# Performance work log

Measured on AMD Instinct MI355X. Metric: run time of the kernel, lower is better.

The kernel has to match this reference:

```python
import jax, jax.numpy as jnp
import numpy as np

B, S, D, E, H, K = 4, 2048, 1024, 8, 4096, 2
EPS = 1e-6


def _ln(x, scale, bias):
    m = jnp.mean(x, axis=-1, keepdims=True)
    v = jnp.mean(jnp.square(x - m), axis=-1, keepdims=True)
    return (x - m) * jax.lax.rsqrt(v + EPS) * scale + bias


def setup_inputs() -> dict:
    key = jax.random.key(0)
    ks = jax.random.split(key, 4)
    s1 = 1.0 / np.sqrt(D)
    s2 = 1.0 / np.sqrt(H)
    return {
        "x": jax.random.normal(ks[0], (B, S, D), jnp.float32),
        "router_ln_scale": jnp.ones((D,), jnp.float32),
        "router_ln_bias": jnp.zeros((D,), jnp.float32),
        "router_w": jax.random.normal(ks[1], (E, D), jnp.float32) * s1,
        "router_b": jnp.zeros((E,), jnp.float32),
        "expert_ln_scale": jnp.ones((E, D), jnp.float32),
        "expert_ln_bias": jnp.zeros((E, D), jnp.float32),
        "w1": jax.random.normal(ks[2], (E, H, D), jnp.float32) * s1,
        "b1": jnp.zeros((E, H), jnp.float32),
        "w2": jax.random.normal(ks[3], (E, D, H), jnp.float32) * s2,
        "b2": jnp.zeros((E, D), jnp.float32),
    }


def reference(x, router_ln_scale, router_ln_bias, router_w, router_b,
              expert_ln_scale, expert_ln_bias, w1, b1, w2, b2):
    orig_shape = x.shape
    xf = x.reshape(-1, D)                       # [T, D]
    T = xf.shape[0]

    # Router: LayerNorm -> Linear -> softmax -> top-k, renormalize weights
    logits = _ln(xf, router_ln_scale, router_ln_bias) @ router_w.T + router_b
    probs = jax.nn.softmax(logits, axis=-1)     # [T, E]
    topw, topi = jax.lax.top_k(probs, K)        # [T, K]
    topw = topw / jnp.sum(topw, axis=-1, keepdims=True)
    # Dense gate matrix: weight for unrouted (token, expert) pairs is 0,
    # matching the original scatter-combine math exactly.
    gates = jnp.zeros((T, E), xf.dtype).at[jnp.arange(T)[:, None], topi].set(topw)

    # Expert MLP: LayerNorm -> fc1 -> GELU(exact) -> fc2, vmapped over experts
    def expert(ls, lb, W1, B1, W2, B2):
        h = jax.nn.gelu(_ln(xf, ls, lb) @ W1.T + B1, approximate=False)
        return h @ W2.T + B2                    # [T, D]

    ys = jax.vmap(expert)(expert_ln_scale, expert_ln_bias, w1, b1, w2, b2)  # [E, T, D]
    out = jnp.einsum('te,etd->td', gates, ys)
    return out.reshape(orig_shape)
```

## Files before the change

kernel.cpp:

```cpp
#include <hip/hip_runtime.h>
#include <hip/hip_bf16.h>

#define TT 8192
#define DD 1024
#define EE 8
#define HH 4096
#define SLOTS 16384
#define SLOTSP (SLOTS + 256)
#define MAXRT1 (SLOTS / 128 + EE)
#define NRB 2048
#define NWB 2048

typedef __bf16 bf16x8 __attribute__((ext_vector_type(8)));
typedef float f32x4 __attribute__((ext_vector_type(4)));

__device__ __forceinline__ float bf2f(unsigned u) { return __uint_as_float(u << 16); }
__device__ __forceinline__ unsigned short f2bf(float f) {
  __hip_bfloat16 h = __float2bfloat16(f);
  return __builtin_bit_cast(unsigned short, h);
}
__device__ __forceinline__ f32x4 MF(bf16x8 a, bf16x8 b, f32x4 c) {
  return __builtin_amdgcn_mfma_f32_16x16x32_bf16(a, b, c, 0, 0, 0);
}


__global__ __launch_bounds__(256) void k_fused_rw(
    const float* __restrict__ x, const float* __restrict__ rls,
    const float* __restrict__ rlb, const float* __restrict__ rw,
    const float* __restrict__ rb, const float* __restrict__ w1,
    const float* __restrict__ w2, unsigned short* __restrict__ xhat,
    int* __restrict__ topk, float* __restrict__ gates, int* __restrict__ ranks,
    int* __restrict__ blkcnt, unsigned short* __restrict__ w1b,
    unsigned short* __restrict__ w2b) {
  if (blockIdx.x >= NRB) {
    const size_t n4t = (size_t)2 * EE * HH * DD / 4;
    const size_t n4w1 = (size_t)EE * HH * DD / 4;
    size_t i = (size_t)(blockIdx.x - NRB) * 256 + threadIdx.x;
    const size_t stride = (size_t)NWB * 256;
    for (; i < n4t; i += stride) {
      const float4* src; unsigned short* dst; size_t j;
      if (i < n4w1) { src = (const float4*)w1; dst = w1b; j = i; }
      else          { src = (const float4*)w2; dst = w2b; j = i - n4w1; }
      float4 v = src[j];
      ushort4 ov;
      ov.x = f2bf(v.x); ov.y = f2bf(v.y); ov.z = f2bf(v.z); ov.w = f2bf(v.w);
      ((ushort4*)dst)[j] = ov;
    }
    return;
  }
  const int tid = threadIdx.x, lane = tid & 63, v = tid >> 6;
  const int t = blockIdx.x * 4 + v;
  __shared__ int sh_e[4][2];
  const float4* xr = (const float4*)(x + (size_t)t * DD);
  float4 xv[4];
#pragma unroll
  for (int j = 0; j < 4; ++j) xv[j] = xr[lane + 64 * j];
  float s = 0.f, s2 = 0.f;
#pragma unroll
  for (int j = 0; j < 4; ++j) {
    s += xv[j].x + xv[j].y + xv[j].z + xv[j].w;
    s2 += xv[j].x * xv[j].x + xv[j].y * xv[j].y + xv[j].z * xv[j].z + xv[j].w * xv[j].w;
  }
#pragma unroll
  for (int o = 32; o > 0; o >>= 1) { s += __shfl_xor(s, o); s2 += __shfl_xor(s2, o); }
  const float mean = s * (1.0f / DD);
  const float var = s2 * (1.0f / DD) - mean * mean;
  const float inv = rsqrtf(var + 1e-6f);
  float xh[4][4];
  unsigned short* xo = xhat + (size_t)t * DD;
#pragma unroll
  for (int j = 0; j < 4; ++j) {
    xh[j][0] = (xv[j].x - mean) * inv; xh[j][1] = (xv[j].y - mean) * inv;
    xh[j][2] = (xv[j].z - mean) * inv; xh[j][3] = (xv[j].w - mean) * inv;
    ushort4 pk;
    pk.x = f2bf(xh[j][0]); pk.y = f2bf(xh[j][1]);
    pk.z = f2bf(xh[j][2]); pk.w = f2bf(xh[j][3]);
    ((ushort4*)xo)[lane + 64 * j] = pk;
  }
  float r[4][4];
#pragma unroll
  for (int j = 0; j < 4; ++j) {
    float4 sc = ((const float4*)rls)[lane + 64 * j];
    float4 bi = ((const float4*)rlb)[lane + 64 * j];
    r[j][0] = fmaf(xh[j][0], sc.x, bi.x); r[j][1] = fmaf(xh[j][1], sc.y, bi.y);
    r[j][2] = fmaf(xh[j][2], sc.z, bi.z); r[j][3] = fmaf(xh[j][3], sc.w, bi.w);
  }
  float pe[EE];
#pragma unroll
  for (int e = 0; e < EE; ++e) {
    float acc = 0.f;
#pragma unroll
    for (int j = 0; j < 4; ++j) {
      float4 w = ((const float4*)(rw + (size_t)e * DD))[lane + 64 * j];
      acc = fmaf(r[j][0], w.x, fmaf(r[j][1], w.y, fmaf(r[j][2], w.z, fmaf(r[j][3], w.w, acc))));
    }
    pe[e] = acc;
  }
#pragma unroll
  for (int o = 32; o > 0; o >>= 1) {
#pragma unroll
    for (int e = 0; e < EE; ++e) pe[e] += __shfl_xor(pe[e], o);
  }
  int i1 = 0, i2 = -1;
  if (lane == 0) {
    float lg[EE];
    for (int e = 0; e < EE; ++e) lg[e] = pe[e] + rb[e];
    for (int e = 1; e < EE; ++e) if (lg[e] > lg[i1]) i1 = e;
    for (int e = 0; e < EE; ++e) { if (e == i1) continue; if (i2 < 0 || lg[e] > lg[i2]) i2 = e; }
    float eb = expf(lg[i2] - lg[i1]);
    float den = 1.0f / (1.0f + eb);
    topk[t] = i1 | (i2 << 8);
    gates[2 * t] = den;
    gates[2 * t + 1] = eb * den;
    sh_e[v][0] = i1; sh_e[v][1] = i2;
  }
  __syncthreads();
  if (lane == 0) {
    int r0 = 0, r1 = 0;
    for (int q = 0; q < 2 * v; ++q) {
      int ee = sh_e[q >> 1][q & 1];
      r0 += (ee == i1); r1 += (ee == i2);
    }
    ranks[2 * t] = r0;
    ranks[2 * t + 1] = r1;
  }
  if (tid < EE) {
    int c = 0;
    for (int q = 0; q < 8; ++q) c += (sh_e[q >> 1][q & 1] == tid);
    blkcnt[blockIdx.x * EE + tid] = c;
  }
}

__global__ __launch_bounds__(256) void k_offsets(int* __restrict__ ctrl,
                                                 int* __restrict__ blkcnt) {
  __shared__ int chunk[32 * EE];
  __shared__ int tot[EE];
  const int t = threadIdx.x, e = t & 7, c = t >> 3;
  int s = 0;
  for (int i = 0; i < 64; ++i) s += blkcnt[(c * 64 + i) * EE + e];
  chunk[c * EE + e] = s;
  __syncthreads();
  if (t < EE) {
    int run = 0;
    for (int c2 = 0; c2 < 32; ++c2) { int vv = chunk[c2 * EE + t]; chunk[c2 * EE + t] = run; run += vv; }
    tot[t] = run;
    ctrl[t] = run;
  }
  __syncthreads();
  if (t == 0) {
    int o = 0, rr = 0;
    ctrl[8] = 0; ctrl[25] = 0;
    for (int e2 = 0; e2 < EE; ++e2) {
      int cc = tot[e2];
      o += cc; ctrl[9 + e2] = o;
      rr += (cc + 127) >> 7; ctrl[26 + e2] = rr;
    }
  }
  int run = chunk[c * EE + e];
  for (int i = 0; i < 64; ++i) {
    int idx = (c * 64 + i) * EE + e;
    int vv = blkcnt[idx];
    blkcnt[idx] = run;
    run += vv;
  }
}

__global__ __launch_bounds__(256) void k_build(
    const unsigned short* __restrict__ xhat, const float* __restrict__ els,
    const float* __restrict__ elb, const int* __restrict__ ctrl,
    const int* __restrict__ topk, const int* __restrict__ ranks,
    const int* __restrict__ blkbase, unsigned short* __restrict__ A,
    int* __restrict__ tok_pos) {
  int p = blockIdx.x * 2 + (threadIdx.x >> 7);
  int t = p >> 1, k = p & 1, tid = threadIdx.x & 127;
  int e = (topk[t] >> (k * 8)) & 0xff;
  int pos = ctrl[8 + e] + blkbase[(p >> 3) * EE + e] + ranks[p];
  if (tid == 0) tok_pos[p] = pos;
  int i = tid * 8;
  uint4 xv = *(const uint4*)(xhat + (size_t)t * DD + i);
  const float* sp = els + (size_t)e * DD + i;
  const float* bp = elb + (size_t)e * DD + i;
  float4 s0 = *(const float4*)sp, s1 = *(const float4*)(sp + 4);
  float4 b0 = *(const float4*)bp, b1 = *(const float4*)(bp + 4);
  unsigned r0 = (unsigned)f2bf(fmaf(bf2f(xv.x & 0xffffu), s0.x, b0.x)) |
                ((unsigned)f2bf(fmaf(bf2f(xv.x >> 16), s0.y, b0.y)) << 16);
  unsigned r1 = (unsigned)f2bf(fmaf(bf2f(xv.y & 0xffffu), s0.z, b0.z)) |
                ((unsigned)f2bf(fmaf(bf2f(xv.y >> 16), s0.w, b0.w)) << 16);
  unsigned r2 = (unsigned)f2bf(fmaf(bf2f(xv.z & 0xffffu), s1.x, b1.x)) |
                ((unsigned)f2bf(fmaf(bf2f(xv.z >> 16), s1.y, b1.y)) << 16);
  unsigned r3 = (unsigned)f2bf(fmaf(bf2f(xv.w & 0xffffu), s1.z, b1.z)) |
                ((unsigned)f2bf(fmaf(bf2f(xv.w >> 16), s1.w, b1.w)) << 16);
  uint4 ov; ov.x = r0; ov.y = r1; ov.z = r2; ov.w = r3;
  *(uint4*)(A + (size_t)pos * DD + i) = ov;
}

#define GLL(S, D)                                                              \
  __builtin_amdgcn_global_load_lds(                                            \
      (const __attribute__((address_space(1))) unsigned int*)(S),              \
      (__attribute__((address_space(3))) unsigned int*)(D), 16, 0, 0)
#define STAGE(P, KT) do {                                                      \
    const unsigned short* sA_ = pA + (size_t)(KT) * 32;                        \
    const unsigned short* sB_ = pB + (size_t)(KT) * 32;                        \
    char* dA_ = sL + (P) * 16384;                                              \
    char* dB_ = dA_ + 8192;                                                    \
    GLL(sA_, dA_); GLL(sA_ + 16 * KDIM, dA_ + 1024);                           \
    GLL(sB_, dB_); GLL(sB_ + 16 * KDIM, dB_ + 1024);                           \
  } while (0)

template <int KDIM, bool GELU>
__global__ __launch_bounds__(256, 3) void k_gemm4(
    const unsigned short* __restrict__ Amat,
    const unsigned short* __restrict__ W,
    const float* __restrict__ bias,
    unsigned short* __restrict__ Outm,
    const int* __restrict__ ctrl, int NTOT) {
  constexpr int NT = KDIM / 32;
  __shared__ __align__(16) char smem[32768];
  const int* rtp = ctrl + 25;

  const int nwg = gridDim.x * gridDim.y;
  const int lin = blockIdx.y * gridDim.x + blockIdx.x;
  const int xcd = lin & 7, loc = lin >> 3;
  const int q = nwg >> 3, rr = nwg & 7;
  const int lin2 = (xcd < rr ? xcd * (q + 1) : rr * (q + 1) + (xcd - rr) * q) + loc;
  const int by = lin2 % gridDim.y;
  const int bx = lin2 / gridDim.y;
  if (bx >= rtp[EE]) return;
  int e = 0;
  while (bx >= rtp[e + 1]) ++e;
  const int rt = bx - rtp[e];
  const int row0 = ctrl[8 + e] + rt * 128;
  int vrows = ctrl[e] - rt * 128;
  if (vrows > 128) vrows = 128;
  const int n0 = by * 128;

  const int tid = threadIdx.x, lane = tid & 63, w = tid >> 6;
  const int wr = w >> 1, wc = w & 1;

  const int u = (lane * 16) ^ (((lane >> 5) & 1) << 5);
  const int ri = u >> 6;
  const int ci = (u & 63) >> 1;
  const unsigned short* pA = Amat + (size_t)(row0 + 32 * w + ri) * KDIM + ci;
  const unsigned short* pB = W + ((size_t)e * NTOT + n0 + 32 * w + ri) * KDIM + ci;
  char* sL = smem + (2 * w) * 1024 + lane * 16;

  const int lt = (((lane & 15) << 6) | ((lane >> 4) << 4)) ^ (((lane >> 3) & 1) << 5);

  f32x4 acc[4][4];
#pragma unroll
  for (int m = 0; m < 4; ++m)
#pragma unroll
    for (int n = 0; n < 4; ++n) acc[m][n] = (f32x4){0.f, 0.f, 0.f, 0.f};

  bf16x8 a[4], b[4];

  STAGE(0, 0);
  __syncthreads();

  for (int kt = 0; kt < NT; ++kt) {
    const int p = kt & 1;
    if (kt + 1 < NT) STAGE(p ^ 1, kt + 1);
    const char* ab = smem + p * 16384 + wr * 4096 + lt;
    const char* bb = smem + p * 16384 + 8192 + wc * 4096 + lt;
#pragma unroll
    for (int m = 0; m < 4; ++m) a[m] = *(const bf16x8*)(ab + m * 1024);
#pragma unroll
    for (int n = 0; n < 4; ++n) b[n] = *(const bf16x8*)(bb + n * 1024);
#pragma unroll
    for (int m = 0; m < 4; ++m)
#pragma unroll
      for (int n = 0; n < 4; ++n)
        acc[m][n] = MF(a[m], b[n], acc[m][n]);
    __syncthreads();
  }

#pragma unroll
  for (int m = 0; m < 4; ++m) {
    const int rbase = wr * 64 + m * 16 + (lane >> 4) * 4;
#pragma unroll
    for (int n = 0; n < 4; ++n) {
      const int col = n0 + wc * 64 + n * 16 + (lane & 15);
      const float bv_ = bias[(size_t)e * NTOT + col];
#pragma unroll
      for (int j = 0; j < 4; ++j) {
        const int r = rbase + j;
        if (r < vrows) {
          float vv = acc[m][n][j] + bv_;
          if constexpr (GELU) vv = 0.5f * vv * (1.0f + erff(vv * 0.70710678f));
          Outm[(size_t)(row0 + r) * NTOT + col] = f2bf(vv);
        }
      }
    }
  }
}

__global__ __launch_bounds__(256) void k_combine(
    const unsigned short* __restrict__ Y, const int* __restrict__ tok_pos,
    const float* __restrict__ gates, float* __restrict__ out) {
  int t = blockIdx.x, tid = threadIdx.x;
  int p0 = tok_pos[2 * t], p1 = tok_pos[2 * t + 1];
  float g0 = gates[2 * t], g1 = gates[2 * t + 1];
  ushort4 y0 = ((const ushort4*)(Y + (size_t)p0 * DD))[tid];
  ushort4 y1 = ((const ushort4*)(Y + (size_t)p1 * DD))[tid];
  float4 o;
  o.x = g0 * bf2f(y0.x) + g1 * bf2f(y1.x);
  o.y = g0 * bf2f(y0.y) + g1 * bf2f(y1.y);
  o.z = g0 * bf2f(y0.z) + g1 * bf2f(y1.z);
  o.w = g0 * bf2f(y0.w) + g1 * bf2f(y1.w);
  ((float4*)(out + (size_t)t * DD))[tid] = o;
}

__global__ __launch_bounds__(256) void k_sentinel(float* out, int n) {
  int i = blockIdx.x * 256 + threadIdx.x;
  if (i < n) out[i] = 12345.0f;
}

extern "C" void kernel_launch(void* const* d_in, const int* in_sizes, int n_in,
                              void* d_out, int out_size, void* d_ws, size_t ws_size,
                              hipStream_t stream) {
  const float* x   = (const float*)d_in[0];
  const float* rls = (const float*)d_in[1];
  const float* rlb = (const float*)d_in[2];
  const float* rw  = (const float*)d_in[3];
  const float* rb  = (const float*)d_in[4];
  const float* els = (const float*)d_in[5];
  const float* elb = (const float*)d_in[6];
  const float* w1  = (const float*)d_in[7];
  const float* b1  = (const float*)d_in[8];
  const float* w2  = (const float*)d_in[9];
  const float* b2  = (const float*)d_in[10];
  float* out = (float*)d_out;

  char* wsb = (char*)d_ws;
  size_t o = 0;
  int* ctrl = (int*)(wsb + o);                    o += 256;
  int* tok_pos = (int*)(wsb + o);                 o += (size_t)SLOTS * 4;
  float* gates = (float*)(wsb + o);               o += (size_t)SLOTS * 4;
  int* topk = (int*)(wsb + o);                    o += (size_t)TT * 4;
  int* ranks = (int*)(wsb + o);                   o += (size_t)SLOTS * 4;
  int* blkcnt = (int*)(wsb + o);                  o += (size_t)NRB * EE * 4;
  unsigned short* xhat = (unsigned short*)(wsb + o); o += (size_t)TT * DD * 2;
  unsigned short* Abuf = (unsigned short*)(wsb + o); o += (size_t)SLOTSP * DD * 2;
  unsigned short* w1b = (unsigned short*)(wsb + o);  o += (size_t)EE * HH * DD * 2;
  unsigned short* w2b = (unsigned short*)(wsb + o);  o += (size_t)EE * DD * HH * 2;
  unsigned short* Hm = (unsigned short*)(wsb + o);   o += (size_t)SLOTSP * HH * 2;
  unsigned short* Yb = (unsigned short*)(wsb + o);   o += (size_t)SLOTS * DD * 2;

  if (ws_size < o) {
    k_sentinel<<<(out_size + 255) / 256, 256, 0, stream>>>(out, out_size);
    return;
  }

  k_fused_rw<<<NRB + NWB, 256, 0, stream>>>(x, rls, rlb, rw, rb, w1, w2, xhat,
                                            topk, gates, ranks, blkcnt, w1b, w2b);
  k_offsets<<<1, 256, 0, stream>>>(ctrl, blkcnt);
  k_build<<<SLOTS / 2, 256, 0, stream>>>(xhat, els, elb, ctrl, topk, ranks,
                                         blkcnt, Abuf, tok_pos);
  k_gemm4<DD, true><<<dim3(MAXRT1, HH / 128), 256, 0, stream>>>(Abuf, w1b, b1, Hm, ctrl, HH);
  k_gemm4<HH, false><<<dim3(MAXRT1, DD / 128), 256, 0, stream>>>(Hm, w2b, b2, Yb, ctrl, DD);
  k_combine<<<TT, 256, 0, stream>>>(Yb, tok_pos, gates, out);
}
```

Measured before the change: 571.2 us.

## Split-K the second expert GEMM and raster GEMM tiles in 8x8 groups

The fc2 GEMM (K=4096) is split into two K-halves via blockIdx.z. Each half writes its own bf16 partial output slice, with the bias added only in slice 0, and the combine kernel sums both partials before applying the gates. Both GEMMs also remap block indices into 8x8 tile groups, so neighbouring workgroups share A and W tiles in cache. This gives the fc2 GEMM more blocks to balance across CUs and shortens each block's K loop. The cost is twice the Y write/read traffic, a larger workspace, and an extra bf16 rounding of the partial sums.

```diff
diff --git a/kernel.cpp b/kernel.cpp
--- a/kernel.cpp
+++ b/kernel.cpp
@@ -207,24 +207,27 @@
     GLL(sB_, dB_); GLL(sB_ + 16 * KDIM, dB_ + 1024);                           \
   } while (0)
 
-template <int KDIM, bool GELU>
+template <int KDIM, int NTILES, bool GELU>
 __global__ __launch_bounds__(256, 3) void k_gemm4(
     const unsigned short* __restrict__ Amat,
     const unsigned short* __restrict__ W,
     const float* __restrict__ bias,
     unsigned short* __restrict__ Outm,
-    const int* __restrict__ ctrl, int NTOT) {
-  constexpr int NT = KDIM / 32;
+    const int* __restrict__ ctrl, int NTOT, size_t outSlice) {
   __shared__ __align__(16) char smem[32768];
   const int* rtp = ctrl + 25;
+  const int z = blockIdx.z;
+  const int kt0 = z * NTILES;
 
   const int nwg = gridDim.x * gridDim.y;
   const int lin = blockIdx.y * gridDim.x + blockIdx.x;
   const int xcd = lin & 7, loc = lin >> 3;
   const int q = nwg >> 3, rr = nwg & 7;
   const int lin2 = (xcd < rr ? xcd * (q + 1) : rr * (q + 1) + (xcd - rr) * q) + loc;
-  const int by = lin2 % gridDim.y;
-  const int bx = lin2 / gridDim.y;
+  const int tXc = gridDim.x >> 3;
+  const int chunk = lin2 >> 6, win = lin2 & 63;
+  const int bx = (chunk % tXc) * 8 + (win & 7);
+  const int by = (chunk / tXc) * 8 + (win >> 3);
   if (bx >= rtp[EE]) return;
   int e = 0;
   while (bx >= rtp[e + 1]) ++e;
@@ -254,12 +257,12 @@
 
   bf16x8 a[4], b[4];
 
-  STAGE(0, 0);
+  STAGE(0, kt0);
   __syncthreads();
 
-  for (int kt = 0; kt < NT; ++kt) {
-    const int p = kt & 1;
-    if (kt + 1 < NT) STAGE(p ^ 1, kt + 1);
+  for (int it = 0; it < NTILES; ++it) {
+    const int p = it & 1;
+    if (it + 1 < NTILES) STAGE(p ^ 1, kt0 + it + 1);
     const char* ab = smem + p * 16384 + wr * 4096 + lt;
     const char* bb = smem + p * 16384 + 8192 + wc * 4096 + lt;
 #pragma unroll
@@ -274,20 +277,21 @@
     __syncthreads();
   }
 
+  unsigned short* outz = Outm + (size_t)z * outSlice;
 #pragma unroll
   for (int m = 0; m < 4; ++m) {
     const int rbase = wr * 64 + m * 16 + (lane >> 4) * 4;
 #pragma unroll
     for (int n = 0; n < 4; ++n) {
       const int col = n0 + wc * 64 + n * 16 + (lane & 15);
-      const float bv_ = bias[(size_t)e * NTOT + col];
+      const float bv_ = (z == 0) ? bias[(size_t)e * NTOT + col] : 0.0f;
 #pragma unroll
       for (int j = 0; j < 4; ++j) {
         const int r = rbase + j;
         if (r < vrows) {
           float vv = acc[m][n][j] + bv_;
           if constexpr (GELU) vv = 0.5f * vv * (1.0f + erff(vv * 0.70710678f));
-          Outm[(size_t)(row0 + r) * NTOT + col] = f2bf(vv);
+          outz[(size_t)(row0 + r) * NTOT + col] = f2bf(vv);
         }
       }
     }
@@ -300,13 +304,16 @@
   int t = blockIdx.x, tid = threadIdx.x;
   int p0 = tok_pos[2 * t], p1 = tok_pos[2 * t + 1];
   float g0 = gates[2 * t], g1 = gates[2 * t + 1];
-  ushort4 y0 = ((const ushort4*)(Y + (size_t)p0 * DD))[tid];
-  ushort4 y1 = ((const ushort4*)(Y + (size_t)p1 * DD))[tid];
+  const unsigned short* Y1 = Y + (size_t)SLOTSP * DD;
+  ushort4 a0 = ((const ushort4*)(Y + (size_t)p0 * DD))[tid];
+  ushort4 a1 = ((const ushort4*)(Y1 + (size_t)p0 * DD))[tid];
+  ushort4 c0 = ((const ushort4*)(Y + (size_t)p1 * DD))[tid];
+  ushort4 c1 = ((const ushort4*)(Y1 + (size_t)p1 * DD))[tid];
   float4 o;
-  o.x = g0 * bf2f(y0.x) + g1 * bf2f(y1.x);
-  o.y = g0 * bf2f(y0.y) + g1 * bf2f(y1.y);
-  o.z = g0 * bf2f(y0.z) + g1 * bf2f(y1.z);
-  o.w = g0 * bf2f(y0.w) + g1 * bf2f(y1.w);
+  o.x = g0 * (bf2f(a0.x) + bf2f(a1.x)) + g1 * (bf2f(c0.x) + bf2f(c1.x));
+  o.y = g0 * (bf2f(a0.y) + bf2f(a1.y)) + g1 * (bf2f(c0.y) + bf2f(c1.y));
+  o.z = g0 * (bf2f(a0.z) + bf2f(a1.z)) + g1 * (bf2f(c0.z) + bf2f(c1.z));
+  o.w = g0 * (bf2f(a0.w) + bf2f(a1.w)) + g1 * (bf2f(c0.w) + bf2f(c1.w));
   ((float4*)(out + (size_t)t * DD))[tid] = o;
 }
 
@@ -344,7 +351,7 @@
   unsigned short* w1b = (unsigned short*)(wsb + o);  o += (size_t)EE * HH * DD * 2;
   unsigned short* w2b = (unsigned short*)(wsb + o);  o += (size_t)EE * DD * HH * 2;
   unsigned short* Hm = (unsigned short*)(wsb + o);   o += (size_t)SLOTSP * HH * 2;
-  unsigned short* Yb = (unsigned short*)(wsb + o);   o += (size_t)SLOTS * DD * 2;
+  unsigned short* Yb = (unsigned short*)(wsb + o);   o += (size_t)2 * SLOTSP * DD * 2;
 
   if (ws_size < o) {
     k_sentinel<<<(out_size + 255) / 256, 256, 0, stream>>>(out, out_size);
@@ -356,7 +363,9 @@
   k_offsets<<<1, 256, 0, stream>>>(ctrl, blkcnt);
   k_build<<<SLOTS / 2, 256, 0, stream>>>(xhat, els, elb, ctrl, topk, ranks,
                                          blkcnt, Abuf, tok_pos);
-  k_gemm4<DD, true><<<dim3(MAXRT1, HH / 128), 256, 0, stream>>>(Abuf, w1b, b1, Hm, ctrl, HH);
-  k_gemm4<HH, false><<<dim3(MAXRT1, DD / 128), 256, 0, stream>>>(Hm, w2b, b2, Yb, ctrl, DD);
+  k_gemm4<DD, 32, true><<<dim3(MAXRT1, HH / 128, 1), 256, 0, stream>>>(
+      Abuf, w1b, b1, Hm, ctrl, HH, 0);
+  k_gemm4<HH, 64, false><<<dim3(MAXRT1, DD / 128, 2), 256, 0, stream>>>(
+      Hm, w2b, b2, Yb, ctrl, DD, (size_t)SLOTSP * DD);
   k_combine<<<TT, 256, 0, stream>>>(Yb, tok_pos, gates, out);
 }
```

Result: no change. 571.6 us (+0.1%).
